# Optimization experiments

Measured on AMD Instinct MI355X. Metric: run time of the kernel, lower is better.

The kernel has to match this reference:

```python
import jax, jax.numpy as jnp
import numpy as np

B, S, H, NH = 16, 512, 768, 12
HD = H // NH


def setup_inputs() -> dict:
    key = jax.random.key(0)
    ks = jax.random.split(key, 8)
    w = 0.02
    return {
        "x": jax.random.normal(ks[0], (B, S, H), jnp.float32),
        "key_padding_mask": jnp.zeros((B, S), jnp.bool_),
        "in_proj_w": jax.random.normal(ks[1], (3 * H, H), jnp.float32) * w,
        "in_proj_b": jnp.zeros((3 * H,), jnp.float32),
        "out_proj_w": jax.random.normal(ks[2], (H, H), jnp.float32) * w,
        "out_proj_b": jnp.zeros((H,), jnp.float32),
        "w1": jax.random.normal(ks[3], (4 * H, H), jnp.float32) * w,
        "b1": jnp.zeros((4 * H,), jnp.float32),
        "w2": jax.random.normal(ks[4], (H, 4 * H), jnp.float32) * w,
        "b2": jnp.zeros((H,), jnp.float32),
        "ln1_g": jnp.ones((H,), jnp.float32),
        "ln1_b": jnp.zeros((H,), jnp.float32),
        "ln2_g": jnp.ones((H,), jnp.float32),
        "ln2_b": jnp.zeros((H,), jnp.float32),
    }


def _layernorm(x, g, b, eps=1e-5):
    m = jnp.mean(x, axis=-1, keepdims=True)
    v = jnp.var(x, axis=-1, keepdims=True)
    return (x - m) / jnp.sqrt(v + eps) * g + b


def reference(x, key_padding_mask, in_proj_w, in_proj_b, out_proj_w, out_proj_b,
              w1, b1, w2, b2, ln1_g, ln1_b, ln2_g, ln2_b):
    b, s, h = x.shape
    # --- nn.MultiheadAttention (batch_first, need_weights, per-head weights) ---
    qkv = x @ in_proj_w.T + in_proj_b                      # [B,S,3H]
    q, k, v = jnp.split(qkv, 3, axis=-1)
    q = q.reshape(b, s, NH, HD).transpose(0, 2, 1, 3)      # [B,NH,S,HD]
    k = k.reshape(b, s, NH, HD).transpose(0, 2, 1, 3)
    v = v.reshape(b, s, NH, HD).transpose(0, 2, 1, 3)
    scale = 1.0 / np.sqrt(HD).astype(np.float32)
    scores = jnp.einsum('bhqd,bhkd->bhqk', q * scale, k)   # [B,NH,S,S]
    scores = jnp.where(key_padding_mask[:, None, None, :], -jnp.inf, scores)
    attn_weights = jax.nn.softmax(scores, axis=-1)         # returned per-head
    attn_out = jnp.einsum('bhqk,bhkd->bhqd', attn_weights, v)
    attn_out = attn_out.transpose(0, 2, 1, 3).reshape(b, s, h)
    attn_out = attn_out @ out_proj_w.T + out_proj_b
    # --- residual + LN, FFN + residual + LN (dropout is identity in eval) ---
    x = _layernorm(x + attn_out, ln1_g, ln1_b)
    ffn = jax.nn.gelu(x @ w1.T + b1, approximate=False) @ w2.T + b2
    x = _layernorm(x + ffn, ln2_g, ln2_b)
    return x, attn_weights
```

## Files before the change

### kernel.cpp

```cpp
#include <hip/hip_runtime.h>
#include <hip/hip_bf16.h>
#include <math.h>

typedef __bf16 bf16;
typedef __attribute__((ext_vector_type(8))) __bf16 bf16x8;
typedef __attribute__((ext_vector_type(4))) __bf16 bf16x4;
typedef __attribute__((ext_vector_type(4))) float f32x4;

#define B_  16
#define S_  512
#define H_  768
#define NH_ 12
#define HD_ 64
#define A_  (B_*S_)

__device__ __forceinline__ void gload_lds16(const void* g, void* l) {
  __builtin_amdgcn_global_load_lds((const __attribute__((address_space(1))) void*)g,
                                   (__attribute__((address_space(3))) void*)l, 16, 0, 0);
}

template<int EPI, int BN_>
__global__ __launch_bounds__(512, 2) void k_gemm(
    const bf16* __restrict__ Amat, const bf16* __restrict__ Bt,
    const float* __restrict__ bias, const bf16* __restrict__ resB,
    bf16* __restrict__ outB,
    bf16* __restrict__ outQ, bf16* __restrict__ outK, bf16* __restrict__ outVT,
    int M, int N, int K)
{
  constexpr int NFRAG  = BN_ / 64;
  constexpr int UNITS  = 2 + NFRAG;
  constexpr int SLOT_E = 8192 + BN_ * 64;
  constexpr int WN     = BN_ / 4;
  __shared__ __align__(16) bf16 LDS[3 * SLOT_E];
  const int tid = threadIdx.x;
  const int w = tid >> 6, l = tid & 63;
  const int lr = l & 15, hi = l >> 4;
  const int wm = w >> 2, wn = w & 3;

  const int nbx = N / BN_;
  const int cpx = gridDim.x >> 3;
  const int sw  = (blockIdx.x & 7) * cpx + (blockIdx.x >> 3);
  const int by = sw / nbx, bx = sw - by * nbx;
  const int row0 = by * 128, col0 = bx * BN_;
  const int NT = K / 64;

  auto stage = [&](int t, int u) {
    bf16* slot = LDS + (t % 3) * SLOT_E;
    if (u < 2) {
      const int fc = u*512 + tid;
      const int r = fc >> 3, s = fc & 7;
      const int gs = s ^ (r & 7);
      gload_lds16(Amat + (size_t)(row0 + r)*K + t*64 + gs*8,
                  slot + (size_t)fc*8 - (size_t)l*8);
    } else {
      const int fc = (u-2)*512 + tid;
      const int r = fc >> 3, s = fc & 7;
      const int gs = s ^ (r & 7);
      gload_lds16(Bt + (size_t)(col0 + r)*K + t*64 + gs*8,
                  slot + 8192 + (size_t)fc*8 - (size_t)l*8);
    }
  };

  f32x4 acc[4][NFRAG] = {};

#pragma unroll
  for (int u = 0; u < UNITS; ++u) stage(0, u);
#pragma unroll
  for (int u = 0; u < UNITS; ++u) stage(1, u);
  if constexpr (UNITS == 5) asm volatile("s_waitcnt vmcnt(5)" ::: "memory");
  else                      asm volatile("s_waitcnt vmcnt(6)" ::: "memory");
  __builtin_amdgcn_s_barrier();

  for (int t = 0; t < NT; ++t) {
    const bf16* slot = LDS + (t % 3) * SLOT_E;
    const bool pre = (t + 2 < NT);

    bf16x8 af[4], bfr[NFRAG];
#pragma unroll
    for (int m = 0; m < 4; ++m) {
      const int r = wm*64 + m*16 + lr;
      af[m] = *(const bf16x8*)(slot + r*64 + (hi ^ (r & 7))*8);
    }
#pragma unroll
    for (int n = 0; n < NFRAG; ++n) {
      const int r = wn*WN + n*16 + lr;
      bfr[n] = *(const bf16x8*)(slot + 8192 + r*64 + (hi ^ (r & 7))*8);
    }
    if (pre) {
      stage(t+2, 0); stage(t+2, 1); stage(t+2, 2);
      if constexpr (UNITS == 6) stage(t+2, 3);
    }
    __builtin_amdgcn_s_barrier();
    asm volatile("s_waitcnt lgkmcnt(0)" ::: "memory");
    __builtin_amdgcn_sched_barrier(0);
    __builtin_amdgcn_s_setprio(1);
#pragma unroll
    for (int m = 0; m < 4; ++m)
#pragma unroll
      for (int n = 0; n < NFRAG; ++n)
        acc[m][n] = __builtin_amdgcn_mfma_f32_16x16x32_bf16(af[m], bfr[n], acc[m][n], 0, 0, 0);
    __builtin_amdgcn_s_setprio(0);
    __builtin_amdgcn_s_barrier();

#pragma unroll
    for (int m = 0; m < 4; ++m) {
      const int r = wm*64 + m*16 + lr;
      af[m] = *(const bf16x8*)(slot + r*64 + ((4 + hi) ^ (r & 7))*8);
    }
#pragma unroll
    for (int n = 0; n < NFRAG; ++n) {
      const int r = wn*WN + n*16 + lr;
      bfr[n] = *(const bf16x8*)(slot + 8192 + r*64 + ((4 + hi) ^ (r & 7))*8);
    }
    if (pre) {
      if constexpr (UNITS == 5) { stage(t+2, 3); stage(t+2, 4); }
      else                      { stage(t+2, 4); stage(t+2, 5); }
    }
    __builtin_amdgcn_s_barrier();
    asm volatile("s_waitcnt lgkmcnt(0)" ::: "memory");
    __builtin_amdgcn_sched_barrier(0);
    __builtin_amdgcn_s_setprio(1);
#pragma unroll
    for (int m = 0; m < 4; ++m)
#pragma unroll
      for (int n = 0; n < NFRAG; ++n)
        acc[m][n] = __builtin_amdgcn_mfma_f32_16x16x32_bf16(af[m], bfr[n], acc[m][n], 0, 0, 0);
    __builtin_amdgcn_s_setprio(0);

    if (t < NT - 1) {
      if (pre) {
        if constexpr (UNITS == 5) asm volatile("s_waitcnt vmcnt(5)" ::: "memory");
        else                      asm volatile("s_waitcnt vmcnt(6)" ::: "memory");
      } else {
        asm volatile("s_waitcnt vmcnt(0)" ::: "memory");
      }
      __builtin_amdgcn_s_barrier();
    }
  }

#pragma unroll
  for (int m = 0; m < 4; ++m) {
#pragma unroll
    for (int n = 0; n < NFRAG; ++n) {
#pragma unroll
      for (int i = 0; i < 4; ++i) {
        const int row = row0 + wm*64 + m*16 + hi*4 + i;
        const int col = col0 + wn*WN + n*16 + lr;
        float v = acc[m][n][i] + bias[col];
        if constexpr (EPI == 2) {
          v = 0.5f * v * (1.0f + erff(v * 0.7071067811865475f));
          outB[(size_t)row*N + col] = (bf16)v;
        } else if constexpr (EPI == 4) {
          v += (float)resB[(size_t)row*N + col];
          outB[(size_t)row*N + col] = (bf16)v;
        } else {
          const int b = row >> 9, s = row & 511;
          const int which = col / H_;
          const int hcol = col - which * H_;
          const int h = hcol >> 6, d = hcol & 63;
          const size_t bh = (size_t)b * NH_ + h;
          if (which == 0)      outQ[(bh*S_ + s)*HD_ + d] = (bf16)v;
          else if (which == 1) outK[(bh*S_ + s)*HD_ + d] = (bf16)v;
          else                 outVT[(bh*HD_ + d)*S_ + s] = (bf16)v;
        }
      }
    }
  }
}

template<int EPI>
__global__ __launch_bounds__(512, 4) void k_gemm_db(
    const bf16* __restrict__ Amat, const bf16* __restrict__ Bt,
    const float* __restrict__ bias, bf16* __restrict__ outB,
    int M, int N, int K)
{
  constexpr int BN_ = 192, NFRAG = 3, SLOT_E = 8192 + BN_*64, WN = 48;
  __shared__ __align__(16) bf16 LDS[2 * SLOT_E];
  const int tid = threadIdx.x;
  const int w = tid >> 6, l = tid & 63;
  const int lr = l & 15, hi = l >> 4;
  const int wm = w >> 2, wn = w & 3;

  const int nbx = N / BN_;
  const int cpx = gridDim.x >> 3;
  const int sw  = (blockIdx.x & 7) * cpx + (blockIdx.x >> 3);
  const int by = sw / nbx, bx = sw - by * nbx;
  const int row0 = by * 128, col0 = bx * BN_;
  const int NT = K / 64;

  auto stage = [&](int t, int u) {
    bf16* slot = LDS + (t & 1) * SLOT_E;
    if (u < 2) {
      const int fc = u*512 + tid;
      const int r = fc >> 3, s = fc & 7;
      const int gs = s ^ (r & 7);
      gload_lds16(Amat + (size_t)(row0 + r)*K + t*64 + gs*8,
                  slot + (size_t)fc*8 - (size_t)l*8);
    } else {
      const int fc = (u-2)*512 + tid;
      const int r = fc >> 3, s = fc & 7;
      const int gs = s ^ (r & 7);
      gload_lds16(Bt + (size_t)(col0 + r)*K + t*64 + gs*8,
                  slot + 8192 + (size_t)fc*8 - (size_t)l*8);
    }
  };

  f32x4 acc[4][NFRAG] = {};

#pragma unroll
  for (int u = 0; u < 5; ++u) stage(0, u);
  asm volatile("s_waitcnt vmcnt(0)" ::: "memory");
  __builtin_amdgcn_s_barrier();

  for (int t = 0; t < NT; ++t) {
    const bf16* slot = LDS + (t & 1) * SLOT_E;
    const bool pre = (t + 1 < NT);

    bf16x8 af[4], bfr[NFRAG];
#pragma unroll
    for (int m = 0; m < 4; ++m) {
      const int r = wm*64 + m*16 + lr;
      af[m] = *(const bf16x8*)(slot + r*64 + (hi ^ (r & 7))*8);
    }
#pragma unroll
    for (int n = 0; n < NFRAG; ++n) {
      const int r = wn*WN + n*16 + lr;
      bfr[n] = *(const bf16x8*)(slot + 8192 + r*64 + (hi ^ (r & 7))*8);
    }
    if (pre) { stage(t+1, 0); stage(t+1, 1); stage(t+1, 2); }
    __builtin_amdgcn_s_barrier();
    asm volatile("s_waitcnt lgkmcnt(0)" ::: "memory");
    __builtin_amdgcn_sched_barrier(0);
    __builtin_amdgcn_s_setprio(1);
#pragma unroll
    for (int m = 0; m < 4; ++m)
#pragma unroll
      for (int n = 0; n < NFRAG; ++n)
        acc[m][n] = __builtin_amdgcn_mfma_f32_16x16x32_bf16(af[m], bfr[n], acc[m][n], 0, 0, 0);
    __builtin_amdgcn_s_setprio(0);
    __builtin_amdgcn_s_barrier();

#pragma unroll
    for (int m = 0; m < 4; ++m) {
      const int r = wm*64 + m*16 + lr;
      af[m] = *(const bf16x8*)(slot + r*64 + ((4 + hi) ^ (r & 7))*8);
    }
#pragma unroll
    for (int n = 0; n < NFRAG; ++n) {
      const int r = wn*WN + n*16 + lr;
      bfr[n] = *(const bf16x8*)(slot + 8192 + r*64 + ((4 + hi) ^ (r & 7))*8);
    }
    if (pre) { stage(t+1, 3); stage(t+1, 4); }
    __builtin_amdgcn_s_barrier();
    asm volatile("s_waitcnt lgkmcnt(0)" ::: "memory");
    __builtin_amdgcn_sched_barrier(0);
    __builtin_amdgcn_s_setprio(1);
#pragma unroll
    for (int m = 0; m < 4; ++m)
#pragma unroll
      for (int n = 0; n < NFRAG; ++n)
        acc[m][n] = __builtin_amdgcn_mfma_f32_16x16x32_bf16(af[m], bfr[n], acc[m][n], 0, 0, 0);
    __builtin_amdgcn_s_setprio(0);

    if (t < NT - 1) {
      asm volatile("s_waitcnt vmcnt(0)" ::: "memory");
      __builtin_amdgcn_s_barrier();
    }
  }

#pragma unroll
  for (int m = 0; m < 4; ++m) {
#pragma unroll
    for (int n = 0; n < NFRAG; ++n) {
#pragma unroll
      for (int i = 0; i < 4; ++i) {
        const int row = row0 + wm*64 + m*16 + hi*4 + i;
        const int col = col0 + wn*WN + n*16 + lr;
        float v = acc[m][n][i] + bias[col];
        v = 0.5f * v * (1.0f + erff(v * 0.7071067811865475f));
        outB[(size_t)row*N + col] = (bf16)v;
      }
    }
  }
}

__global__ __launch_bounds__(256) void k_attn_fused(
    const bf16* __restrict__ Qm, const bf16* __restrict__ Km, const bf16* __restrict__ VT,
    const unsigned char* __restrict__ mask, float* __restrict__ P, bf16* __restrict__ AO)
{
  __shared__ __align__(16) bf16 KVs[512*64];
  const int tid = threadIdx.x, w = tid >> 6, l = tid & 63;
  const int lr = l & 15, hi = l >> 4;
  const int cpx = gridDim.x >> 3;
  const int sw  = (blockIdx.x & 7) * cpx + (blockIdx.x >> 3);
  const int bh = sw >> 3, qt = sw & 7;
  const int b = bh / NH_, h = bh - b * NH_;
  const int swz = (lr & 7) << 4;

  const bf16* Kg = Km + (size_t)bh * S_ * HD_;
#pragma unroll
  for (int rnd = 0; rnd < 16; ++rnd) {
    const int c = rnd*256 + tid;
    const int row = c >> 3, col16 = (c & 7) ^ (row & 7);
    gload_lds16(Kg + row*HD_ + col16*8, KVs + (rnd*4 + w)*512);
  }
  const bf16* qrow_g = Qm + (size_t)bh * S_ * HD_ + (size_t)(qt*64 + w*16 + lr) * HD_;
  bf16x8 qf0 = *(const bf16x8*)(qrow_g + hi*8);
  bf16x8 qf1 = *(const bf16x8*)(qrow_g + 32 + hi*8);
  __syncthreads();

  f32x4 acc[32];
#pragma unroll
  for (int ct = 0; ct < 32; ++ct) acc[ct] = f32x4{0.f,0.f,0.f,0.f};
#pragma unroll
  for (int ct = 0; ct < 32; ++ct) {
    const char* kb = (const char*)(KVs + (ct*16 + lr)*64);
    bf16x8 a0 = *(const bf16x8*)(kb + ((hi*16) ^ swz));
    bf16x8 a1 = *(const bf16x8*)(kb + ((64 + hi*16) ^ swz));
    acc[ct] = __builtin_amdgcn_mfma_f32_16x16x32_bf16(a0, qf0, acc[ct], 0, 0, 0);
    acc[ct] = __builtin_amdgcn_mfma_f32_16x16x32_bf16(a1, qf1, acc[ct], 0, 0, 0);
  }
  __syncthreads();

  const bf16* Vg = VT + (size_t)bh * HD_ * S_;
#pragma unroll
  for (int rnd = 0; rnd < 16; ++rnd) {
    const int c = rnd*256 + tid;
    const int row = c >> 6, col16 = (c & 63) ^ (row & 7);
    gload_lds16(Vg + row*S_ + col16*8, KVs + (rnd*4 + w)*512);
  }

  const unsigned char* mrow = mask + b * S_;
  float mx = -1e30f;
#pragma unroll
  for (int ct = 0; ct < 32; ++ct) {
    const unsigned mk4 = *(const unsigned*)(mrow + ct*16 + hi*4);
#pragma unroll
    for (int i = 0; i < 4; ++i) {
      float v = acc[ct][i] * 0.125f;
      if ((mk4 >> (8*i)) & 0xff) v = -1e30f;
      acc[ct][i] = v;
      mx = fmaxf(mx, v);
    }
  }
  mx = fmaxf(mx, __shfl_xor(mx, 16));
  mx = fmaxf(mx, __shfl_xor(mx, 32));
  float sum = 0.f;
#pragma unroll
  for (int ct = 0; ct < 32; ++ct)
#pragma unroll
    for (int i = 0; i < 4; ++i) { float e = __expf(acc[ct][i] - mx); acc[ct][i] = e; sum += e; }
  sum += __shfl_xor(sum, 16);
  sum += __shfl_xor(sum, 32);
  const float inv = 1.f / sum;

  float* prow = P + ((size_t)bh*S_ + (size_t)qt*64 + w*16 + lr) * S_;
#pragma unroll
  for (int ct = 0; ct < 32; ++ct) {
#pragma unroll
    for (int i = 0; i < 4; ++i) acc[ct][i] *= inv;
    __builtin_nontemporal_store(acc[ct], (f32x4*)(prow + ct*16 + hi*4));
  }
  __syncthreads();

  f32x4 o[4] = {};
#pragma unroll
  for (int c = 0; c < 16; ++c) {
    bf16x8 pa;
#pragma unroll
    for (int i = 0; i < 4; ++i) { pa[i] = (bf16)acc[2*c][i]; pa[4+i] = (bf16)acc[2*c+1][i]; }
    const int cb0 = (64*c + 8*hi) ^ swz;
    const int cb1 = (64*c + 32 + 8*hi) ^ swz;
#pragma unroll
    for (int nt = 0; nt < 4; ++nt) {
      const char* vb = (const char*)(KVs + (nt*16 + lr)*512);
      bf16x4 v0 = *(const bf16x4*)(vb + cb0);
      bf16x4 v1 = *(const bf16x4*)(vb + cb1);
      bf16x8 vf = {v0[0],v0[1],v0[2],v0[3], v1[0],v1[1],v1[2],v1[3]};
      o[nt] = __builtin_amdgcn_mfma_f32_16x16x32_bf16(pa, vf, o[nt], 0, 0, 0);
    }
  }

  bf16* aorow = AO + ((size_t)(b*S_ + qt*64 + w*16))*H_ + h*HD_;
#pragma unroll
  for (int nt = 0; nt < 4; ++nt)
#pragma unroll
    for (int i = 0; i < 4; ++i)
      aorow[(size_t)(hi*4 + i)*H_ + nt*16 + lr] = (bf16)o[nt][i];
}

__global__ __launch_bounds__(256) void k_layernorm(
    const bf16* __restrict__ X, const float* __restrict__ g, const float* __restrict__ bta,
    float* __restrict__ outF, bf16* __restrict__ outB)
{
  const int w = threadIdx.x >> 6, l = threadIdx.x & 63;
  const int row = blockIdx.x * 4 + w;
  const bf16* x = X + (size_t)row * H_;
  float v[12]; float s = 0.f, ss = 0.f;
#pragma unroll
  for (int j = 0; j < 3; ++j) {
    bf16x4 b4 = *(const bf16x4*)(x + l*4 + j*256);
#pragma unroll
    for (int e = 0; e < 4; ++e) {
      const float f = (float)b4[e];
      v[j*4 + e] = f; s += f; ss += f*f;
    }
  }
#pragma unroll
  for (int d = 1; d < 64; d <<= 1) { s += __shfl_xor(s, d); ss += __shfl_xor(ss, d); }
  const float mean = s * (1.f / H_);
  const float var  = ss * (1.f / H_) - mean * mean;
  const float inv  = rsqrtf(var + 1e-5f);
#pragma unroll
  for (int j = 0; j < 3; ++j) {
    const int c = l*4 + j*256;
    const float4 gv = *(const float4*)(g + c);
    const float4 bv = *(const float4*)(bta + c);
    f32x4 y;
    y[0] = (v[j*4+0] - mean)*inv*gv.x + bv.x;
    y[1] = (v[j*4+1] - mean)*inv*gv.y + bv.y;
    y[2] = (v[j*4+2] - mean)*inv*gv.z + bv.z;
    y[3] = (v[j*4+3] - mean)*inv*gv.w + bv.w;
    if (outF) __builtin_nontemporal_store(y, (f32x4*)(outF + (size_t)row*H_ + c));
    if (outB) {
      bf16x4 o; o[0]=(bf16)y[0]; o[1]=(bf16)y[1]; o[2]=(bf16)y[2]; o[3]=(bf16)y[3];
      *(bf16x4*)(outB + (size_t)row*H_ + c) = o;
    }
  }
}

#define NB0 (A_*H_/1024)
#define NB1 (3*H_*H_/1024)
#define NB2 (H_*H_/1024)
#define NB3 (4*H_*H_/1024)
#define NB4 (4*H_*H_/1024)
__global__ void k_conv_all(
    const float* __restrict__ s0, bf16* __restrict__ d0,
    const float* __restrict__ s1, bf16* __restrict__ d1,
    const float* __restrict__ s2, bf16* __restrict__ d2,
    const float* __restrict__ s3, bf16* __restrict__ d3,
    const float* __restrict__ s4, bf16* __restrict__ d4)
{
  int b = blockIdx.x;
  const float* src; bf16* dst;
  if      (b < NB0)                   { src = s0; dst = d0; }
  else if ((b -= NB0) < NB1)          { src = s1; dst = d1; }
  else if ((b -= NB1) < NB2)          { src = s2; dst = d2; }
  else if ((b -= NB2) < NB3)          { src = s3; dst = d3; }
  else    { b -= NB3;                   src = s4; dst = d4; }
  const int i = (b * 256 + threadIdx.x) * 4;
  const float4 vv = *(const float4*)(src + i);
  bf16x4 o; o[0]=(bf16)vv.x; o[1]=(bf16)vv.y; o[2]=(bf16)vv.z; o[3]=(bf16)vv.w;
  *(bf16x4*)(dst + i) = o;
}

extern "C" void kernel_launch(void* const* d_in, const int* in_sizes, int n_in,
                              void* d_out, int out_size, void* d_ws, size_t ws_size,
                              hipStream_t stream) {
  const float* x      = (const float*)d_in[0];
  const unsigned char* mask = (const unsigned char*)d_in[1];
  const float* w_qkv  = (const float*)d_in[2];
  const float* b_qkv  = (const float*)d_in[3];
  const float* w_out  = (const float*)d_in[4];
  const float* b_out  = (const float*)d_in[5];
  const float* w1     = (const float*)d_in[6];
  const float* b1     = (const float*)d_in[7];
  const float* w2     = (const float*)d_in[8];
  const float* b2     = (const float*)d_in[9];
  const float* ln1g   = (const float*)d_in[10];
  const float* ln1b   = (const float*)d_in[11];
  const float* ln2g   = (const float*)d_in[12];
  const float* ln2b   = (const float*)d_in[13];

  float* xout = (float*)d_out;
  float* P    = xout + (size_t)A_ * H_;

  char* ws = (char*)d_ws;
  size_t off = 0;
  auto alloc = [&](size_t bytes) { char* p = ws + off; off += (bytes + 255) & ~255ull; return p; };

  bf16* xb   = (bf16*)alloc((size_t)A_*H_*2);
  bf16* wqkv = (bf16*)alloc((size_t)3*H_*H_*2);
  bf16* wo   = (bf16*)alloc((size_t)H_*H_*2);
  bf16* w1b  = (bf16*)alloc((size_t)4*H_*H_*2);
  bf16* w2b  = (bf16*)alloc((size_t)4*H_*H_*2);
  char* qreg = alloc((size_t)A_*H_*2*4);
  bf16* q  = (bf16*)qreg;
  bf16* kb = q  + (size_t)A_*H_;
  bf16* vt = kb + (size_t)A_*H_;
  bf16* ao = vt + (size_t)A_*H_;
  bf16* hbuf = q;
  bf16* y1b = (bf16*)alloc((size_t)A_*H_*2);
  bf16* y2b = (bf16*)alloc((size_t)A_*H_*2);
  bf16* x1b = (bf16*)alloc((size_t)A_*H_*2);

  k_conv_all<<<NB0+NB1+NB2+NB3+NB4, 256, 0, stream>>>(
      x, xb, w_qkv, wqkv, w_out, wo, w1, w1b, w2, w2b);

  k_gemm<0,192><<<(A_/128)*(3*H_/192), 512, 0, stream>>>(xb, wqkv, b_qkv, nullptr,
      nullptr, q, kb, vt, A_, 3*H_, H_);
  k_attn_fused<<<B_*NH_*8, 256, 0, stream>>>(q, kb, vt, mask, P, ao);
  k_gemm<4,192><<<(A_/128)*(H_/192), 512, 0, stream>>>(ao, wo, b_out, xb,
      y1b, nullptr, nullptr, nullptr, A_, H_, H_);
  k_layernorm<<<A_/4, 256, 0, stream>>>(y1b, ln1g, ln1b, nullptr, x1b);
  k_gemm_db<2><<<(A_/128)*(4*H_/192), 512, 0, stream>>>(x1b, w1b, b1,
      hbuf, A_, 4*H_, H_);
  k_gemm<4,192><<<(A_/128)*(H_/192), 512, 0, stream>>>(hbuf, w2b, b2, x1b,
      y2b, nullptr, nullptr, nullptr, A_, H_, 4*H_);
  k_layernorm<<<A_/4, 256, 0, stream>>>(y2b, ln2g, ln2b, xout, nullptr);
}
```

Measured before the change: 304.0 us.

## Split-K the FFN2 GEMM and fuse partial reduction into final layernorm

The FFN down-projection (K=3072) now runs as a two-way split-K on the double-buffered, 4-blocks-per-CU GEMM. Each K-slice writes fp32 partials, and a new layernorm kernel sums the partials, bias and residual before normalizing. This doubles the block count for the narrow N=768 GEMM to improve CU occupancy, and drops the bf16 y2b intermediate. The QKV projection also moves from the triple-buffered GEMM to the double-buffered, higher-occupancy kernel. In exchange it adds extra fp32 partial traffic of roughly 2x A*H*4 bytes.

```diff
diff --git a/kernel.cpp b/kernel.cpp
--- a/kernel.cpp
+++ b/kernel.cpp
@@ -19,18 +19,14 @@
                                    (__attribute__((address_space(3))) void*)l, 16, 0, 0);
 }
 
-template<int EPI, int BN_>
+template<int EPI>
 __global__ __launch_bounds__(512, 2) void k_gemm(
     const bf16* __restrict__ Amat, const bf16* __restrict__ Bt,
     const float* __restrict__ bias, const bf16* __restrict__ resB,
     bf16* __restrict__ outB,
-    bf16* __restrict__ outQ, bf16* __restrict__ outK, bf16* __restrict__ outVT,
     int M, int N, int K)
 {
-  constexpr int NFRAG  = BN_ / 64;
-  constexpr int UNITS  = 2 + NFRAG;
-  constexpr int SLOT_E = 8192 + BN_ * 64;
-  constexpr int WN     = BN_ / 4;
+  constexpr int BN_ = 192, NFRAG = 3, UNITS = 5, SLOT_E = 8192 + BN_*64, WN = 48;
   __shared__ __align__(16) bf16 LDS[3 * SLOT_E];
   const int tid = threadIdx.x;
   const int w = tid >> 6, l = tid & 63;
@@ -67,8 +63,7 @@
   for (int u = 0; u < UNITS; ++u) stage(0, u);
 #pragma unroll
   for (int u = 0; u < UNITS; ++u) stage(1, u);
-  if constexpr (UNITS == 5) asm volatile("s_waitcnt vmcnt(5)" ::: "memory");
-  else                      asm volatile("s_waitcnt vmcnt(6)" ::: "memory");
+  asm volatile("s_waitcnt vmcnt(5)" ::: "memory");
   __builtin_amdgcn_s_barrier();
 
   for (int t = 0; t < NT; ++t) {
@@ -86,10 +81,7 @@
       const int r = wn*WN + n*16 + lr;
       bfr[n] = *(const bf16x8*)(slot + 8192 + r*64 + (hi ^ (r & 7))*8);
     }
-    if (pre) {
-      stage(t+2, 0); stage(t+2, 1); stage(t+2, 2);
-      if constexpr (UNITS == 6) stage(t+2, 3);
-    }
+    if (pre) { stage(t+2, 0); stage(t+2, 1); stage(t+2, 2); }
     __builtin_amdgcn_s_barrier();
     asm volatile("s_waitcnt lgkmcnt(0)" ::: "memory");
     __builtin_amdgcn_sched_barrier(0);
@@ -112,10 +104,7 @@
       const int r = wn*WN + n*16 + lr;
       bfr[n] = *(const bf16x8*)(slot + 8192 + r*64 + ((4 + hi) ^ (r & 7))*8);
     }
-    if (pre) {
-      if constexpr (UNITS == 5) { stage(t+2, 3); stage(t+2, 4); }
-      else                      { stage(t+2, 4); stage(t+2, 5); }
-    }
+    if (pre) { stage(t+2, 3); stage(t+2, 4); }
     __builtin_amdgcn_s_barrier();
     asm volatile("s_waitcnt lgkmcnt(0)" ::: "memory");
     __builtin_amdgcn_sched_barrier(0);
@@ -128,12 +117,8 @@
     __builtin_amdgcn_s_setprio(0);
 
     if (t < NT - 1) {
-      if (pre) {
-        if constexpr (UNITS == 5) asm volatile("s_waitcnt vmcnt(5)" ::: "memory");
-        else                      asm volatile("s_waitcnt vmcnt(6)" ::: "memory");
-      } else {
-        asm volatile("s_waitcnt vmcnt(0)" ::: "memory");
-      }
+      if (pre) asm volatile("s_waitcnt vmcnt(5)" ::: "memory");
+      else     asm volatile("s_waitcnt vmcnt(0)" ::: "memory");
       __builtin_amdgcn_s_barrier();
     }
   }
@@ -147,13 +132,136 @@
         const int row = row0 + wm*64 + m*16 + hi*4 + i;
         const int col = col0 + wn*WN + n*16 + lr;
         float v = acc[m][n][i] + bias[col];
-        if constexpr (EPI == 2) {
+        v += (float)resB[(size_t)row*N + col];
+        outB[(size_t)row*N + col] = (bf16)v;
+      }
+    }
+  }
+}
+
+template<int EPI, int SPLIT>
+__global__ __launch_bounds__(512, 4) void k_gemm_db(
+    const bf16* __restrict__ Amat, const bf16* __restrict__ Bt,
+    const float* __restrict__ bias,
+    bf16* __restrict__ outB, float* __restrict__ outF,
+    bf16* __restrict__ outQ, bf16* __restrict__ outK, bf16* __restrict__ outVT,
+    int M, int N, int Kstride)
+{
+  constexpr int BN_ = 192, NFRAG = 3, SLOT_E = 8192 + BN_*64, WN = 48;
+  __shared__ __align__(16) bf16 LDS[2 * SLOT_E];
+  const int tid = threadIdx.x;
+  const int w = tid >> 6, l = tid & 63;
+  const int lr = l & 15, hi = l >> 4;
+  const int wm = w >> 2, wn = w & 3;
+
+  const int nbx = N / BN_;
+  const int cpx = gridDim.x >> 3;
+  const int sw  = (blockIdx.x & 7) * cpx + (blockIdx.x >> 3);
+  const int tile  = sw >> SPLIT;
+  const int slice = sw & ((1 << SPLIT) - 1);
+  const int by = tile / nbx, bx = tile - by * nbx;
+  const int row0 = by * 128, col0 = bx * BN_;
+  const int Klen = Kstride >> SPLIT;
+  const int koff = slice * Klen;
+  const int NT = Klen / 64;
+
+  auto stage = [&](int t, int u) {
+    bf16* slot = LDS + (t & 1) * SLOT_E;
+    if (u < 2) {
+      const int fc = u*512 + tid;
+      const int r = fc >> 3, s = fc & 7;
+      const int gs = s ^ (r & 7);
+      gload_lds16(Amat + (size_t)(row0 + r)*Kstride + koff + t*64 + gs*8,
+                  slot + (size_t)fc*8 - (size_t)l*8);
+    } else {
+      const int fc = (u-2)*512 + tid;
+      const int r = fc >> 3, s = fc & 7;
+      const int gs = s ^ (r & 7);
+      gload_lds16(Bt + (size_t)(col0 + r)*Kstride + koff + t*64 + gs*8,
+                  slot + 8192 + (size_t)fc*8 - (size_t)l*8);
+    }
+  };
+
+  f32x4 acc[4][NFRAG] = {};
+
+#pragma unroll
+  for (int u = 0; u < 5; ++u) stage(0, u);
+  asm volatile("s_waitcnt vmcnt(0)" ::: "memory");
+  __builtin_amdgcn_s_barrier();
+
+  for (int t = 0; t < NT; ++t) {
+    const bf16* slot = LDS + (t & 1) * SLOT_E;
+    const bool pre = (t + 1 < NT);
+
+    bf16x8 af[4], bfr[NFRAG];
+#pragma unroll
+    for (int m = 0; m < 4; ++m) {
+      const int r = wm*64 + m*16 + lr;
+      af[m] = *(const bf16x8*)(slot + r*64 + (hi ^ (r & 7))*8);
+    }
+#pragma unroll
+    for (int n = 0; n < NFRAG; ++n) {
+      const int r = wn*WN + n*16 + lr;
+      bfr[n] = *(const bf16x8*)(slot + 8192 + r*64 + (hi ^ (r & 7))*8);
+    }
+    if (pre) { stage(t+1, 0); stage(t+1, 1); stage(t+1, 2); }
+    __builtin_amdgcn_s_barrier();
+    asm volatile("s_waitcnt lgkmcnt(0)" ::: "memory");
+    __builtin_amdgcn_sched_barrier(0);
+    __builtin_amdgcn_s_setprio(1);
+#pragma unroll
+    for (int m = 0; m < 4; ++m)
+#pragma unroll
+      for (int n = 0; n < NFRAG; ++n)
+        acc[m][n] = __builtin_amdgcn_mfma_f32_16x16x32_bf16(af[m], bfr[n], acc[m][n], 0, 0, 0);
+    __builtin_amdgcn_s_setprio(0);
+    __builtin_amdgcn_s_barrier();
+
+#pragma unroll
+    for (int m = 0; m < 4; ++m) {
+      const int r = wm*64 + m*16 + lr;
+      af[m] = *(const bf16x8*)(slot + r*64 + ((4 + hi) ^ (r & 7))*8);
+    }
+#pragma unroll
+    for (int n = 0; n < NFRAG; ++n) {
+      const int r = wn*WN + n*16 + lr;
+      bfr[n] = *(const bf16x8*)(slot + 8192 + r*64 + ((4 + hi) ^ (r & 7))*8);
+    }
+    if (pre) { stage(t+1, 3); stage(t+1, 4); }
+    __builtin_amdgcn_s_barrier();
+    asm volatile("s_waitcnt lgkmcnt(0)" ::: "memory");
+    __builtin_amdgcn_sched_barrier(0);
+    __builtin_amdgcn_s_setprio(1);
+#pragma unroll
+    for (int m = 0; m < 4; ++m)
+#pragma unroll
+      for (int n = 0; n < NFRAG; ++n)
+        acc[m][n] = __builtin_amdgcn_mfma_f32_16x16x32_bf16(af[m], bfr[n], acc[m][n], 0, 0, 0);
+    __builtin_amdgcn_s_setprio(0);
+
+    if (t < NT - 1) {
+      asm volatile("s_waitcnt vmcnt(0)" ::: "memory");
+      __builtin_amdgcn_s_barrier();
+    }
+  }
+
+#pragma unroll
+  for (int m = 0; m < 4; ++m) {
+#pragma unroll
+    for (int n = 0; n < NFRAG; ++n) {
+#pragma unroll
+      for (int i = 0; i < 4; ++i) {
+        const int row = row0 + wm*64 + m*16 + hi*4 + i;
+        const int col = col0 + wn*WN + n*16 + lr;
+        if constexpr (EPI == 5) {
+          __builtin_nontemporal_store(acc[m][n][i],
+              outF + (size_t)slice*M*N + (size_t)row*N + col);
+        } else if constexpr (EPI == 2) {
+          float v = acc[m][n][i] + bias[col];
           v = 0.5f * v * (1.0f + erff(v * 0.7071067811865475f));
           outB[(size_t)row*N + col] = (bf16)v;
-        } else if constexpr (EPI == 4) {
-          v += (float)resB[(size_t)row*N + col];
-          outB[(size_t)row*N + col] = (bf16)v;
         } else {
+          float v = acc[m][n][i] + bias[col];
           const int b = row >> 9, s = row & 511;
           const int which = col / H_;
           const int hcol = col - which * H_;
@@ -163,122 +271,6 @@
           else if (which == 1) outK[(bh*S_ + s)*HD_ + d] = (bf16)v;
           else                 outVT[(bh*HD_ + d)*S_ + s] = (bf16)v;
         }
-      }
-    }
-  }
-}
-
-template<int EPI>
-__global__ __launch_bounds__(512, 4) void k_gemm_db(
-    const bf16* __restrict__ Amat, const bf16* __restrict__ Bt,
-    const float* __restrict__ bias, bf16* __restrict__ outB,
-    int M, int N, int K)
-{
-  constexpr int BN_ = 192, NFRAG = 3, SLOT_E = 8192 + BN_*64, WN = 48;
-  __shared__ __align__(16) bf16 LDS[2 * SLOT_E];
-  const int tid = threadIdx.x;
-  const int w = tid >> 6, l = tid & 63;
-  const int lr = l & 15, hi = l >> 4;
-  const int wm = w >> 2, wn = w & 3;
-
-  const int nbx = N / BN_;
-  const int cpx = gridDim.x >> 3;
-  const int sw  = (blockIdx.x & 7) * cpx + (blockIdx.x >> 3);
-  const int by = sw / nbx, bx = sw - by * nbx;
-  const int row0 = by * 128, col0 = bx * BN_;
-  const int NT = K / 64;
-
-  auto stage = [&](int t, int u) {
-    bf16* slot = LDS + (t & 1) * SLOT_E;
-    if (u < 2) {
-      const int fc = u*512 + tid;
-      const int r = fc >> 3, s = fc & 7;
-      const int gs = s ^ (r & 7);
-      gload_lds16(Amat + (size_t)(row0 + r)*K + t*64 + gs*8,
-                  slot + (size_t)fc*8 - (size_t)l*8);
-    } else {
-      const int fc = (u-2)*512 + tid;
-      const int r = fc >> 3, s = fc & 7;
-      const int gs = s ^ (r & 7);
-      gload_lds16(Bt + (size_t)(col0 + r)*K + t*64 + gs*8,
-                  slot + 8192 + (size_t)fc*8 - (size_t)l*8);
-    }
-  };
-
-  f32x4 acc[4][NFRAG] = {};
-
-#pragma unroll
-  for (int u = 0; u < 5; ++u) stage(0, u);
-  asm volatile("s_waitcnt vmcnt(0)" ::: "memory");
-  __builtin_amdgcn_s_barrier();
-
-  for (int t = 0; t < NT; ++t) {
-    const bf16* slot = LDS + (t & 1) * SLOT_E;
-    const bool pre = (t + 1 < NT);
-
-    bf16x8 af[4], bfr[NFRAG];
-#pragma unroll
-    for (int m = 0; m < 4; ++m) {
-      const int r = wm*64 + m*16 + lr;
-      af[m] = *(const bf16x8*)(slot + r*64 + (hi ^ (r & 7))*8);
-    }
-#pragma unroll
-    for (int n = 0; n < NFRAG; ++n) {
-      const int r = wn*WN + n*16 + lr;
-      bfr[n] = *(const bf16x8*)(slot + 8192 + r*64 + (hi ^ (r & 7))*8);
-    }
-    if (pre) { stage(t+1, 0); stage(t+1, 1); stage(t+1, 2); }
-    __builtin_amdgcn_s_barrier();
-    asm volatile("s_waitcnt lgkmcnt(0)" ::: "memory");
-    __builtin_amdgcn_sched_barrier(0);
-    __builtin_amdgcn_s_setprio(1);
-#pragma unroll
-    for (int m = 0; m < 4; ++m)
-#pragma unroll
-      for (int n = 0; n < NFRAG; ++n)
-        acc[m][n] = __builtin_amdgcn_mfma_f32_16x16x32_bf16(af[m], bfr[n], acc[m][n], 0, 0, 0);
-    __builtin_amdgcn_s_setprio(0);
-    __builtin_amdgcn_s_barrier();
-
-#pragma unroll
-    for (int m = 0; m < 4; ++m) {
-      const int r = wm*64 + m*16 + lr;
-      af[m] = *(const bf16x8*)(slot + r*64 + ((4 + hi) ^ (r & 7))*8);
-    }
-#pragma unroll
-    for (int n = 0; n < NFRAG; ++n) {
-      const int r = wn*WN + n*16 + lr;
-      bfr[n] = *(const bf16x8*)(slot + 8192 + r*64 + ((4 + hi) ^ (r & 7))*8);
-    }
-    if (pre) { stage(t+1, 3); stage(t+1, 4); }
-    __builtin_amdgcn_s_barrier();
-    asm volatile("s_waitcnt lgkmcnt(0)" ::: "memory");
-    __builtin_amdgcn_sched_barrier(0);
-    __builtin_amdgcn_s_setprio(1);
-#pragma unroll
-    for (int m = 0; m < 4; ++m)
-#pragma unroll
-      for (int n = 0; n < NFRAG; ++n)
-        acc[m][n] = __builtin_amdgcn_mfma_f32_16x16x32_bf16(af[m], bfr[n], acc[m][n], 0, 0, 0);
-    __builtin_amdgcn_s_setprio(0);
-
-    if (t < NT - 1) {
-      asm volatile("s_waitcnt vmcnt(0)" ::: "memory");
-      __builtin_amdgcn_s_barrier();
-    }
-  }
-
-#pragma unroll
-  for (int m = 0; m < 4; ++m) {
-#pragma unroll
-    for (int n = 0; n < NFRAG; ++n) {
-#pragma unroll
-      for (int i = 0; i < 4; ++i) {
-        const int row = row0 + wm*64 + m*16 + hi*4 + i;
-        const int col = col0 + wn*WN + n*16 + lr;
-        float v = acc[m][n][i] + bias[col];
-        v = 0.5f * v * (1.0f + erff(v * 0.7071067811865475f));
-        outB[(size_t)row*N + col] = (bf16)v;
       }
     }
   }
@@ -391,7 +383,7 @@
 
 __global__ __launch_bounds__(256) void k_layernorm(
     const bf16* __restrict__ X, const float* __restrict__ g, const float* __restrict__ bta,
-    float* __restrict__ outF, bf16* __restrict__ outB)
+    bf16* __restrict__ outB)
 {
   const int w = threadIdx.x >> 6, l = threadIdx.x & 63;
   const int row = blockIdx.x * 4 + w;
@@ -405,6 +397,49 @@
       const float f = (float)b4[e];
       v[j*4 + e] = f; s += f; ss += f*f;
     }
+  }
+#pragma unroll
+  for (int d = 1; d < 64; d <<= 1) { s += __shfl_xor(s, d); ss += __shfl_xor(ss, d); }
+  const float mean = s * (1.f / H_);
+  const float var  = ss * (1.f / H_) - mean * mean;
+  const float inv  = rsqrtf(var + 1e-5f);
+#pragma unroll
+  for (int j = 0; j < 3; ++j) {
+    const int c = l*4 + j*256;
+    const float4 gv = *(const float4*)(g + c);
+    const float4 bv = *(const float4*)(bta + c);
+    bf16x4 o;
+    o[0] = (bf16)((v[j*4+0] - mean)*inv*gv.x + bv.x);
+    o[1] = (bf16)((v[j*4+1] - mean)*inv*gv.y + bv.y);
+    o[2] = (bf16)((v[j*4+2] - mean)*inv*gv.z + bv.z);
+    o[3] = (bf16)((v[j*4+3] - mean)*inv*gv.w + bv.w);
+    *(bf16x4*)(outB + (size_t)row*H_ + c) = o;
+  }
+}
+
+__global__ __launch_bounds__(256) void k_ln_ffn2(
+    const float* __restrict__ p0, const float* __restrict__ p1,
+    const float* __restrict__ b2, const bf16* __restrict__ res,
+    const float* __restrict__ g, const float* __restrict__ bta,
+    float* __restrict__ xout)
+{
+  const int w = threadIdx.x >> 6, l = threadIdx.x & 63;
+  const int row = blockIdx.x * 4 + w;
+  const size_t base = (size_t)row * H_;
+  float v[12]; float s = 0.f, ss = 0.f;
+#pragma unroll
+  for (int j = 0; j < 3; ++j) {
+    const int c = l*4 + j*256;
+    const float4 a0 = *(const float4*)(p0 + base + c);
+    const float4 a1 = *(const float4*)(p1 + base + c);
+    const float4 bb = *(const float4*)(b2 + c);
+    bf16x4 r4 = *(const bf16x4*)(res + base + c);
+    v[j*4+0] = a0.x + a1.x + bb.x + (float)r4[0];
+    v[j*4+1] = a0.y + a1.y + bb.y + (float)r4[1];
+    v[j*4+2] = a0.z + a1.z + bb.z + (float)r4[2];
+    v[j*4+3] = a0.w + a1.w + bb.w + (float)r4[3];
+#pragma unroll
+    for (int e = 0; e < 4; ++e) { s += v[j*4+e]; ss += v[j*4+e]*v[j*4+e]; }
   }
 #pragma unroll
   for (int d = 1; d < 64; d <<= 1) { s += __shfl_xor(s, d); ss += __shfl_xor(ss, d); }
@@ -421,11 +456,7 @@
     y[1] = (v[j*4+1] - mean)*inv*gv.y + bv.y;
     y[2] = (v[j*4+2] - mean)*inv*gv.z + bv.z;
     y[3] = (v[j*4+3] - mean)*inv*gv.w + bv.w;
-    if (outF) __builtin_nontemporal_store(y, (f32x4*)(outF + (size_t)row*H_ + c));
-    if (outB) {
-      bf16x4 o; o[0]=(bf16)y[0]; o[1]=(bf16)y[1]; o[2]=(bf16)y[2]; o[3]=(bf16)y[3];
-      *(bf16x4*)(outB + (size_t)row*H_ + c) = o;
-    }
+    __builtin_nontemporal_store(y, (f32x4*)(xout + base + c));
   }
 }
 
@@ -491,21 +522,22 @@
   bf16* ao = vt + (size_t)A_*H_;
   bf16* hbuf = q;
   bf16* y1b = (bf16*)alloc((size_t)A_*H_*2);
-  bf16* y2b = (bf16*)alloc((size_t)A_*H_*2);
   bf16* x1b = (bf16*)alloc((size_t)A_*H_*2);
+  float* part = (float*)alloc((size_t)2*A_*H_*4);
 
   k_conv_all<<<NB0+NB1+NB2+NB3+NB4, 256, 0, stream>>>(
       x, xb, w_qkv, wqkv, w_out, wo, w1, w1b, w2, w2b);
 
-  k_gemm<0,192><<<(A_/128)*(3*H_/192), 512, 0, stream>>>(xb, wqkv, b_qkv, nullptr,
-      nullptr, q, kb, vt, A_, 3*H_, H_);
+  k_gemm_db<0,0><<<(A_/128)*(3*H_/192), 512, 0, stream>>>(xb, wqkv, b_qkv,
+      nullptr, nullptr, q, kb, vt, A_, 3*H_, H_);
   k_attn_fused<<<B_*NH_*8, 256, 0, stream>>>(q, kb, vt, mask, P, ao);
-  k_gemm<4,192><<<(A_/128)*(H_/192), 512, 0, stream>>>(ao, wo, b_out, xb,
-      y1b, nullptr, nullptr, nullptr, A_, H_, H_);
-  k_layernorm<<<A_/4, 256, 0, stream>>>(y1b, ln1g, ln1b, nullptr, x1b);
-  k_gemm_db<2><<<(A_/128)*(4*H_/192), 512, 0, stream>>>(x1b, w1b, b1,
-      hbuf, A_, 4*H_, H_);
-  k_gemm<4,192><<<(A_/128)*(H_/192), 512, 0, stream>>>(hbuf, w2b, b2, x1b,
-      y2b, nullptr, nullptr, nullptr, A_, H_, 4*H_);
-  k_layernorm<<<A_/4, 256, 0, stream>>>(y2b, ln2g, ln2b, xout, nullptr);
-}
+  k_gemm<4><<<(A_/128)*(H_/192), 512, 0, stream>>>(ao, wo, b_out, xb,
+      y1b, A_, H_, H_);
+  k_layernorm<<<A_/4, 256, 0, stream>>>(y1b, ln1g, ln1b, x1b);
+  k_gemm_db<2,0><<<(A_/128)*(4*H_/192), 512, 0, stream>>>(x1b, w1b, b1,
+      hbuf, nullptr, nullptr, nullptr, nullptr, A_, 4*H_, H_);
+  k_gemm_db<5,1><<<(A_/128)*(H_/192)*2, 512, 0, stream>>>(hbuf, w2b, nullptr,
+      nullptr, part, nullptr, nullptr, nullptr, A_, H_, 4*H_);
+  k_ln_ffn2<<<A_/4, 256, 0, stream>>>(part, part + (size_t)A_*H_, b2, x1b,
+      ln2g, ln2b, xout);
+}
```

Result: no change. 298.4 us (-1.8%).
